# Kernel tuning notes

Measured on AMD Instinct MI355X. Metric: run time of the kernel, lower is better.

Reference implementation:

```python
import jax, jax.numpy as jnp
import numpy as np

EMB_DIM = 1024
N_HEADS = 16
HEAD_DIM = EMB_DIM // N_HEADS
B, T = 2, 2048


def setup_inputs() -> dict:
    key = jax.random.key(0)
    ks = jax.random.split(key, 5)
    scale = 1.0 / np.sqrt(EMB_DIM)
    x = jax.random.normal(ks[0], (B, T, EMB_DIM), dtype=jnp.float32)
    # causal mask: True means masked (as in torch masked_fill)
    mask = jnp.triu(jnp.ones((T, T), dtype=bool), k=1)[None, None, :, :]
    WQ = jax.random.normal(ks[1], (EMB_DIM, EMB_DIM), dtype=jnp.float32) * scale
    WK = jax.random.normal(ks[2], (EMB_DIM, EMB_DIM), dtype=jnp.float32) * scale
    WV = jax.random.normal(ks[3], (EMB_DIM, EMB_DIM), dtype=jnp.float32) * scale
    WO = jax.random.normal(ks[4], (EMB_DIM, EMB_DIM), dtype=jnp.float32) * scale
    return {"x": x, "mask": mask, "WQ": WQ, "WK": WK, "WV": WV, "WO": WO}


def reference(x, mask, WQ, WK, WV, WO):
    Bb, Tt, E = x.shape
    H, D = N_HEADS, HEAD_DIM

    def split(y):  # [B,T,E] -> [B,H,T,D]
        return y.reshape(Bb, Tt, H, D).transpose(0, 2, 1, 3)

    # nn.Linear(bias=False): y = x @ W.T with W of shape [out, in]
    Q = split(jnp.einsum('bte,oe->bto', x, WQ))
    K = split(jnp.einsum('bte,oe->bto', x, WK))
    V = split(jnp.einsum('bte,oe->bto', x, WV))

    scores = jnp.einsum('bhqd,bhkd->bhqk', Q, K) / jnp.sqrt(jnp.float32(D))
    scores = jnp.where(mask, -jnp.inf, scores)
    w = jax.nn.softmax(scores, axis=-1)
    w = jnp.nan_to_num(w, nan=0.0)  # fully-masked rows -> 0, as in torch
    out = jnp.einsum('bhqk,bhkd->bhqd', w, V)
    # dropout is identity at inference (eval mode)
    merged = out.transpose(0, 2, 1, 3).reshape(Bb, Tt, E)
    y = jnp.einsum('bte,oe->bto', merged, WO)
    return y, w
```

## Files before the change

kernel.cpp:

```cpp
#include <hip/hip_runtime.h>
#include <cstdint>
#include <cstddef>

typedef __attribute__((ext_vector_type(4))) float  f32x4;
typedef __attribute__((ext_vector_type(8))) short  s16x8;
typedef __attribute__((ext_vector_type(4))) short  s16x4;
typedef __attribute__((ext_vector_type(2))) unsigned int u32x2;

#define EMB   1024
#define NHEAD 16
#define HD    64
#define NB    2
#define TT    2048
#define TQKV  3072

#define C_EXP2 0.18033688011112042f

__device__ __forceinline__ short f2bf(float f) {
  union { float f; unsigned u; } x; x.f = f;
  unsigned r = x.u + 0x7FFFu + ((x.u >> 16) & 1u);
  return (short)(r >> 16);
}

__device__ __forceinline__ unsigned cvt_pk_bf16(float lo, float hi) {
  unsigned r;
  asm("v_cvt_pk_bf16_f32 %0, %1, %2" : "=v"(r) : "v"(lo), "v"(hi));
  return r;
}

__device__ __forceinline__ void gload_lds16(const short* g, short* l) {
  __builtin_amdgcn_global_load_lds(
      (const __attribute__((address_space(1))) void*)(g),
      (__attribute__((address_space(3))) void*)(l), 16, 0, 0);
}

__device__ __forceinline__ void bar_vm0() {
  asm volatile("s_waitcnt vmcnt(0)" ::: "memory");
  __builtin_amdgcn_sched_barrier(0);
  __builtin_amdgcn_s_barrier();
  __builtin_amdgcn_sched_barrier(0);
}
__device__ __forceinline__ void bar_vm1() {
  asm volatile("s_waitcnt vmcnt(1)" ::: "memory");
  __builtin_amdgcn_sched_barrier(0);
  __builtin_amdgcn_s_barrier();
  __builtin_amdgcn_sched_barrier(0);
}
__device__ __forceinline__ void bar_vm4() {
  asm volatile("s_waitcnt vmcnt(4)" ::: "memory");
  __builtin_amdgcn_sched_barrier(0);
  __builtin_amdgcn_s_barrier();
  __builtin_amdgcn_sched_barrier(0);
}

__global__ __launch_bounds__(256) void cvt_all(
    const float* __restrict__ x,  const float* __restrict__ wq,
    const float* __restrict__ wk, const float* __restrict__ wv,
    const float* __restrict__ wo,
    short* __restrict__ xb, short* __restrict__ wqkv, short* __restrict__ wob) {
  int i = blockIdx.x * 256 + threadIdx.x;
  const float* s; short* d; int off;
  if (i < 1048576) { s = x; d = xb; off = i; }
  else {
    int j = i - 1048576;
    int r = j >> 18;
    off = j & 262143;
    s = (r == 0) ? wq : (r == 1) ? wk : (r == 2) ? wv : wo;
    d = (r == 3) ? wob : wqkv + (size_t)r * 1048576;
  }
  f32x4 v = ((const f32x4*)s)[off];
  s16x4 o;
  o[0] = f2bf(v[0]); o[1] = f2bf(v[1]); o[2] = f2bf(v[2]); o[3] = f2bf(v[3]);
  ((s16x4*)d)[off] = o;
}

template <int OUT_BF16>
__global__ __launch_bounds__(512) void gemm_nt(const short* __restrict__ A,
                                               const short* __restrict__ B,
                                               void* __restrict__ C,
                                               int M, int N, int K) {
  __shared__ short lA[2][128 * 32];
  __shared__ short lB[2][128 * 32];
  const int tid  = threadIdx.x;
  const int lane = tid & 63;
  const int wid  = tid >> 6;
  const int bm = blockIdx.y, bn = blockIdx.x;
  const int wm = wid >> 2, wn = wid & 3;

  f32x4 acc[4][2];
#pragma unroll
  for (int i = 0; i < 4; ++i)
#pragma unroll
    for (int j = 0; j < 2; ++j) acc[i][j] = (f32x4){0.f, 0.f, 0.f, 0.f};

  const short* Ab = A + (size_t)bm * 128 * K;
  const short* Bb = B + (size_t)bn * 128 * K;
  const int srow = tid >> 2;
  const int scol = (((tid & 3) ^ (srow & 3))) * 8;

#define G_STAGE(buf, k0)                                                     \
  do {                                                                       \
    gload_lds16(Ab + (size_t)srow * K + (k0) + scol, &lA[buf][tid * 8]);     \
    gload_lds16(Bb + (size_t)srow * K + (k0) + scol, &lB[buf][tid * 8]);     \
  } while (0)

  G_STAGE(0, 0);
  int cur = 0;
  for (int k0 = 0; k0 < K; k0 += 32) {
    __syncthreads();
    if (k0 + 32 < K) G_STAGE(cur ^ 1, k0 + 32);

    s16x8 af[4], bf_[2];
#pragma unroll
    for (int i = 0; i < 4; ++i) {
      const int ra = wm * 64 + i * 16 + (lane & 15);
      af[i] = *(const s16x8*)(&lA[cur][ra * 32 + (((lane >> 4) ^ (ra & 3)) << 3)]);
    }
#pragma unroll
    for (int j = 0; j < 2; ++j) {
      const int rb = wn * 32 + j * 16 + (lane & 15);
      bf_[j] = *(const s16x8*)(&lB[cur][rb * 32 + (((lane >> 4) ^ (rb & 3)) << 3)]);
    }
#pragma unroll
    for (int i = 0; i < 4; ++i)
#pragma unroll
      for (int j = 0; j < 2; ++j)
        acc[i][j] = __builtin_amdgcn_mfma_f32_16x16x32_bf16(af[i], bf_[j], acc[i][j], 0, 0, 0);
    cur ^= 1;
  }
#undef G_STAGE

  const int row0 = bm * 128 + wm * 64;
  const int col0 = bn * 128 + wn * 32;
#pragma unroll
  for (int i = 0; i < 4; ++i)
#pragma unroll
    for (int j = 0; j < 2; ++j)
#pragma unroll
      for (int r = 0; r < 4; ++r) {
        int row = row0 + i * 16 + ((lane >> 4) << 2) + r;
        int col = col0 + j * 16 + (lane & 15);
        float v = acc[i][j][r];
        if (OUT_BF16) ((short*)C)[(size_t)row * N + col] = f2bf(v);
        else          ((float*)C)[(size_t)row * N + col] = v;
      }
}

__global__ __launch_bounds__(256) void transpose_v(const short* __restrict__ qkv,
                                                   short* __restrict__ vt) {
  __shared__ short tile[64 * 72];
  const int tt = blockIdx.x, bh = blockIdx.y;
  const int b = bh >> 4, h = bh & 15;
  const int tid = threadIdx.x;

  const short* src = qkv + ((size_t)(b * TT + tt * 64)) * TQKV + 2048 + h * HD;
#pragma unroll
  for (int p = 0; p < 2; ++p) {
    int r = p * 32 + (tid >> 3);
    int c = (tid & 7) * 8;
    s16x8 v = *(const s16x8*)(src + (size_t)r * TQKV + c);
#pragma unroll
    for (int j = 0; j < 8; ++j) tile[r * 72 + c + j] = v[j];
  }
  __syncthreads();
  short* dst = vt + ((size_t)bh * HD) * TT + tt * 64;
#pragma unroll
  for (int p = 0; p < 2; ++p) {
    int d0 = p * 32 + (tid >> 3);
    int c  = (tid & 7) * 8;
    s16x8 o;
#pragma unroll
    for (int j = 0; j < 8; ++j) o[j] = tile[(c + j) * 72 + d0];
    *(s16x8*)(dst + (size_t)d0 * TT + c) = o;
  }
}

__global__ __launch_bounds__(512) void attn_fused(const short* __restrict__ qkv,
                                                  const short* __restrict__ vt,
                                                  float* __restrict__ wout,
                                                  short* __restrict__ merged) {
  __shared__ short smem[28672];
  short* const lW  = smem;
  short* const lK0 = smem + 8192;
  short* const lK1 = smem + 12288;
  short* const lK2 = smem + 16384;
  short* const lV0 = smem + 20480;
  short* const lV1 = smem + 24576;

  const int tid = threadIdx.x, lane = tid & 63, wid = tid >> 6;
  const int bh = blockIdx.y;
  const int qt = (blockIdx.y < 16) ? (15 - blockIdx.x) : blockIdx.x;
  const int b = bh >> 4, h = bh & 15;
  const int NT = 2 * qt + 2;

  const int srow = tid >> 3;
  const int scol = ((tid & 7) ^ (srow & 7)) * 8;
  const int q15  = lane & 15;
  const int fcs  = (lane >> 4) * 8;
  const int kg4  = (lane >> 4) << 2;
  const int qg   = wid * 16 + q15;
  const int qglob = qt * 128 + qg;
  const int sw   = (q15 & 7) << 3;
  const int qsub = (lane >> 4) << 2;
  const int qrow = qt * 128 + wid * 16 + qsub;
  const int wave_qmin = qt * 128 + wid * 16;

  const short* ksrc0 = qkv + (size_t)(b * TT) * TQKV + EMB + h * HD;
  const short* vsrc0 = vt + (size_t)bh * HD * TT;

#define STAGE_K(dst, kt)                                                       \
  gload_lds16(ksrc0 + (size_t)((kt) * 64 + srow) * TQKV + scol, (dst) + tid * 8)
#define STAGE_V(dst, kt)                                                       \
  gload_lds16(vsrc0 + (size_t)srow * TT + (kt) * 64 + scol,     (dst) + tid * 8)

  const short* qsrc = qkv + ((size_t)(b * TT + qt * 128)) * TQKV + h * HD;
  gload_lds16(qsrc + (size_t)srow * TQKV + scol,        lW + tid * 8);
  gload_lds16(qsrc + (size_t)(srow + 64) * TQKV + scol, lW + 4096 + tid * 8);
  __syncthreads();

  s16x8 aq[2];
  aq[0] = *(const s16x8*)(lW + qg * 64 + ((fcs)      ^ ((qg & 7) << 3)));
  aq[1] = *(const s16x8*)(lW + qg * 64 + ((32 + fcs) ^ ((qg & 7) << 3)));

  float lsum = 0.f;
  {
    short *p0 = lK0, *p1 = lK1, *p2 = lK2;
    STAGE_K(p0, 0);
    STAGE_K(p1, 1);
    bar_vm0();
    for (int kt = 0; kt < NT; ++kt) {
      const bool pre = (kt + 2 < NT);
      if (pre) STAGE_K(p2, kt + 2);

      f32x4 s2[4];
#pragma unroll
      for (int kg = 0; kg < 4; ++kg) s2[kg] = (f32x4){0.f, 0.f, 0.f, 0.f};
#pragma unroll
      for (int ks2 = 0; ks2 < 2; ++ks2)
#pragma unroll
        for (int kg = 0; kg < 4; ++kg) {
          s16x8 bk = *(const s16x8*)(p0 + (kg * 16 + q15) * 64 + ((ks2 * 32 + fcs) ^ sw));
          s2[kg] = __builtin_amdgcn_mfma_f32_16x16x32_bf16(bk, aq[ks2], s2[kg], 0, 0, 0);
        }

      const bool full = (kt * 64 + 63 <= wave_qmin);
      const int kb0 = kt * 64 + kg4;
#pragma unroll
      for (int kg = 0; kg < 4; ++kg)
#pragma unroll
        for (int r = 0; r < 4; ++r) {
          float e = exp2f(s2[kg][r] * C_EXP2);
          if (!full) e = (kb0 + kg * 16 + r <= qglob) ? e : 0.f;
          lsum += e;
        }

      if (pre) bar_vm1();
      else     bar_vm0();
      short* t_ = p0; p0 = p1; p1 = p2; p2 = t_;
    }
  }
  lsum += __shfl_xor(lsum, 16);
  lsum += __shfl_xor(lsum, 32);
  const float lrl = -log2f(lsum);

  f32x4 o[4];
#pragma unroll
  for (int nj = 0; nj < 4; ++nj) o[nj] = (f32x4){0.f, 0.f, 0.f, 0.f};

  {
    short *kc_ = lK0, *kn_ = lK1, *vc_ = lV0, *vn_ = lV1;
    STAGE_K(kc_, 0);
    STAGE_V(vc_, 0);
    bar_vm0();
    float* const wq_base = wout + ((size_t)bh * TT + qglob) * TT;
    for (int kt = 0; kt < NT; ++kt) {
      f32x4 s2[4];
#pragma unroll
      for (int kg = 0; kg < 4; ++kg) s2[kg] = (f32x4){0.f, 0.f, 0.f, 0.f};
#pragma unroll
      for (int ks2 = 0; ks2 < 2; ++ks2)
#pragma unroll
        for (int kg = 0; kg < 4; ++kg) {
          s16x8 bk = *(const s16x8*)(kc_ + (kg * 16 + q15) * 64 + ((ks2 * 32 + fcs) ^ sw));
          s2[kg] = __builtin_amdgcn_mfma_f32_16x16x32_bf16(bk, aq[ks2], s2[kg], 0, 0, 0);
        }

      const bool pre = (kt + 1 < NT);
      if (pre) { STAGE_K(kn_, kt + 1); STAGE_V(vn_, kt + 1); }
      __builtin_amdgcn_sched_barrier(0);

      const bool full = (kt * 64 + 63 <= wave_qmin);
      float* wbase = wq_base + kt * 64 + kg4;
#pragma unroll
      for (int kg = 0; kg < 4; ++kg) {
        f32x4 w4;
#pragma unroll
        for (int r = 0; r < 4; ++r) {
          float e = exp2f(fmaf(s2[kg][r], C_EXP2, lrl));
          w4[r] = (full || (kt * 64 + kg * 16 + kg4 + r <= qglob)) ? e : 0.f;
        }
        *(f32x4*)(wbase + kg * 16) = w4;
        u32x2 pk2;
        pk2.x = cvt_pk_bf16(w4[0], w4[1]);
        pk2.y = cvt_pk_bf16(w4[2], w4[3]);
        const int col = kg * 16 + kg4;
        *(u32x2*)(lW + qg * 64 + (col ^ sw)) = pk2;
      }
      __builtin_amdgcn_sched_barrier(0);

#pragma unroll
      for (int ks2 = 0; ks2 < 2; ++ks2) {
        s16x8 aw = *(const s16x8*)(lW + qg * 64 + ((ks2 * 32 + fcs) ^ ((qg & 7) << 3)));
#pragma unroll
        for (int nj = 0; nj < 4; ++nj) {
          s16x8 bv = *(const s16x8*)(vc_ + (nj * 16 + q15) * 64 + ((ks2 * 32 + fcs) ^ sw));
          o[nj] = __builtin_amdgcn_mfma_f32_16x16x32_bf16(aw, bv, o[nj], 0, 0, 0);
        }
      }

      if (pre) {
        bar_vm4();
        short* t_;
        t_ = kc_; kc_ = kn_; kn_ = t_;
        t_ = vc_; vc_ = vn_; vn_ = t_;
      }
    }
  }
#undef STAGE_K
#undef STAGE_V

#pragma unroll
  for (int nj = 0; nj < 4; ++nj)
#pragma unroll
    for (int r = 0; r < 4; ++r)
      merged[(size_t)(b * TT + qrow + r) * EMB + h * HD + nj * 16 + q15] = f2bf(o[nj][r]);

  {
    const int zrow = tid >> 2, zc = (tid & 3) * 16;
    float* zbase = wout + ((size_t)bh * TT + qt * 128 + zrow) * TT + zc;
    const f32x4 z = (f32x4){0.f, 0.f, 0.f, 0.f};
    for (int kt = NT; kt < TT / 64; ++kt) {
      float* p = zbase + kt * 64;
      *(f32x4*)(p)      = z;
      *(f32x4*)(p + 4)  = z;
      *(f32x4*)(p + 8)  = z;
      *(f32x4*)(p + 12) = z;
    }
  }
}

extern "C" void kernel_launch(void* const* d_in, const int* in_sizes, int n_in,
                              void* d_out, int out_size, void* d_ws, size_t ws_size,
                              hipStream_t stream) {
  const float* x  = (const float*)d_in[0];
  const float* WQ = (const float*)d_in[2];
  const float* WK = (const float*)d_in[3];
  const float* WV = (const float*)d_in[4];
  const float* WO = (const float*)d_in[5];

  float* y    = (float*)d_out;
  float* wout = (float*)d_out + (size_t)NB * TT * EMB;

  char* ws = (char*)d_ws;
  short* xb     = (short*)(ws + 0);
  short* wqkv   = (short*)(ws + 8388608);
  short* wob    = (short*)(ws + 14680064);
  short* qkvb   = (short*)(ws + 16777216);
  short* vtb    = (short*)(ws + 41943040);
  short* merged = (short*)(ws + 50331648);

  cvt_all<<<8192, 256, 0, stream>>>(x, WQ, WK, WV, WO, xb, wqkv, wob);

  gemm_nt<1><<<dim3(24, 32), 512, 0, stream>>>(xb, wqkv, qkvb, 4096, 3072, 1024);

  transpose_v<<<dim3(32, 32), 256, 0, stream>>>(qkvb, vtb);

  attn_fused<<<dim3(16, 32), 512, 0, stream>>>(qkvb, vtb, wout, merged);

  gemm_nt<0><<<dim3(8, 32), 512, 0, stream>>>(merged, wob, y, 4096, 1024, 1024);
}
```

Measured before the change: 241.3 us.

## Process K/V tiles in pairs per barrier with deeper LDS buffering and setprio

Both attention passes now handle two 64-key tiles per loop iteration. LDS grows from three K and two V buffers to eight tile buffers, so that work is staged a pair at a time and each block hits half as many s_barrier and vmcnt waits. MFMA sections are wrapped in s_setprio to favour matrix issue across waves. In exchange, LDS use per block rises, which may cut occupancy. The waitcnt thresholds (vm2/vm4/vm8) depend on the order in which loads and stores retire, so the pipeline depth actually achieved may be smaller than intended.

```diff
diff --git a/kernel.cpp b/kernel.cpp
--- a/kernel.cpp
+++ b/kernel.cpp
@@ -34,24 +34,18 @@
       (__attribute__((address_space(3))) void*)(l), 16, 0, 0);
 }
 
-__device__ __forceinline__ void bar_vm0() {
-  asm volatile("s_waitcnt vmcnt(0)" ::: "memory");
-  __builtin_amdgcn_sched_barrier(0);
-  __builtin_amdgcn_s_barrier();
-  __builtin_amdgcn_sched_barrier(0);
-}
-__device__ __forceinline__ void bar_vm1() {
-  asm volatile("s_waitcnt vmcnt(1)" ::: "memory");
-  __builtin_amdgcn_sched_barrier(0);
-  __builtin_amdgcn_s_barrier();
-  __builtin_amdgcn_sched_barrier(0);
-}
-__device__ __forceinline__ void bar_vm4() {
-  asm volatile("s_waitcnt vmcnt(4)" ::: "memory");
-  __builtin_amdgcn_sched_barrier(0);
-  __builtin_amdgcn_s_barrier();
-  __builtin_amdgcn_sched_barrier(0);
-}
+#define MAKE_BAR(NAME, N)                                          \
+  __device__ __forceinline__ void NAME() {                         \
+    asm volatile("s_waitcnt vmcnt(" #N ")" ::: "memory");          \
+    __builtin_amdgcn_sched_barrier(0);                             \
+    __builtin_amdgcn_s_barrier();                                  \
+    __builtin_amdgcn_sched_barrier(0);                             \
+  }
+MAKE_BAR(bar_vm0, 0)
+MAKE_BAR(bar_vm2, 2)
+MAKE_BAR(bar_vm4, 4)
+MAKE_BAR(bar_vm8, 8)
+#undef MAKE_BAR
 
 __global__ __launch_bounds__(256) void cvt_all(
     const float* __restrict__ x,  const float* __restrict__ wq,
@@ -179,19 +173,16 @@
                                                   const short* __restrict__ vt,
                                                   float* __restrict__ wout,
                                                   short* __restrict__ merged) {
-  __shared__ short smem[28672];
-  short* const lW  = smem;
-  short* const lK0 = smem + 8192;
-  short* const lK1 = smem + 12288;
-  short* const lK2 = smem + 16384;
-  short* const lV0 = smem + 20480;
-  short* const lV1 = smem + 24576;
+  __shared__ short smem[40960];
+  short* const lW    = smem;
+  short* const tiles = smem + 8192;
+#define TB(i) (tiles + (i) * 4096)
 
   const int tid = threadIdx.x, lane = tid & 63, wid = tid >> 6;
   const int bh = blockIdx.y;
   const int qt = (blockIdx.y < 16) ? (15 - blockIdx.x) : blockIdx.x;
   const int b = bh >> 4, h = bh & 15;
-  const int NT = 2 * qt + 2;
+  const int npairs = qt + 1;
 
   const int srow = tid >> 3;
   const int scol = ((tid & 7) ^ (srow & 7)) * 8;
@@ -222,41 +213,55 @@
   aq[0] = *(const s16x8*)(lW + qg * 64 + ((fcs)      ^ ((qg & 7) << 3)));
   aq[1] = *(const s16x8*)(lW + qg * 64 + ((32 + fcs) ^ ((qg & 7) << 3)));
 
+#define QK_TILE(s2v, Kb)                                                       \
+  do {                                                                         \
+    _Pragma("unroll")                                                          \
+    for (int kg = 0; kg < 4; ++kg) s2v[kg] = (f32x4){0.f, 0.f, 0.f, 0.f};      \
+    __builtin_amdgcn_s_setprio(1);                                             \
+    _Pragma("unroll")                                                          \
+    for (int ks2 = 0; ks2 < 2; ++ks2)                                          \
+      _Pragma("unroll")                                                        \
+      for (int kg = 0; kg < 4; ++kg) {                                         \
+        s16x8 bk = *(const s16x8*)((Kb) + (kg * 16 + q15) * 64 +               \
+                                   ((ks2 * 32 + fcs) ^ sw));                   \
+        s2v[kg] = __builtin_amdgcn_mfma_f32_16x16x32_bf16(bk, aq[ks2],         \
+                                                          s2v[kg], 0, 0, 0);   \
+      }                                                                        \
+    __builtin_amdgcn_s_setprio(0);                                             \
+  } while (0)
+
   float lsum = 0.f;
   {
-    short *p0 = lK0, *p1 = lK1, *p2 = lK2;
-    STAGE_K(p0, 0);
-    STAGE_K(p1, 1);
-    bar_vm0();
-    for (int kt = 0; kt < NT; ++kt) {
-      const bool pre = (kt + 2 < NT);
-      if (pre) STAGE_K(p2, kt + 2);
-
-      f32x4 s2[4];
-#pragma unroll
-      for (int kg = 0; kg < 4; ++kg) s2[kg] = (f32x4){0.f, 0.f, 0.f, 0.f};
-#pragma unroll
-      for (int ks2 = 0; ks2 < 2; ++ks2)
-#pragma unroll
-        for (int kg = 0; kg < 4; ++kg) {
-          s16x8 bk = *(const s16x8*)(p0 + (kg * 16 + q15) * 64 + ((ks2 * 32 + fcs) ^ sw));
-          s2[kg] = __builtin_amdgcn_mfma_f32_16x16x32_bf16(bk, aq[ks2], s2[kg], 0, 0, 0);
-        }
-
-      const bool full = (kt * 64 + 63 <= wave_qmin);
-      const int kb0 = kt * 64 + kg4;
-#pragma unroll
-      for (int kg = 0; kg < 4; ++kg)
-#pragma unroll
-        for (int r = 0; r < 4; ++r) {
-          float e = exp2f(s2[kg][r] * C_EXP2);
-          if (!full) e = (kb0 + kg * 16 + r <= qglob) ? e : 0.f;
-          lsum += e;
-        }
-
-      if (pre) bar_vm1();
-      else     bar_vm0();
-      short* t_ = p0; p0 = p1; p1 = p2; p2 = t_;
+    STAGE_K(TB(0), 0); STAGE_K(TB(1), 1);
+    if (npairs > 1) { STAGE_K(TB(2), 2); STAGE_K(TB(3), 3); }
+    if (npairs > 1) bar_vm2(); else bar_vm0();
+    for (int p = 0; p < npairs; ++p) {
+      const int s = p & 3;
+      const bool pre = (p + 2 < npairs);
+      if (pre) {
+        const int sn = (p + 2) & 3;
+        STAGE_K(TB(2 * sn),     2 * p + 4);
+        STAGE_K(TB(2 * sn + 1), 2 * p + 5);
+      }
+      __builtin_amdgcn_sched_barrier(0);
+#pragma unroll
+      for (int u = 0; u < 2; ++u) {
+        const int t = 2 * p + u;
+        const short* Kb = TB(2 * s + u);
+        f32x4 s2v[4];
+        QK_TILE(s2v, Kb);
+        const bool full = (t * 64 + 63 <= wave_qmin);
+        const int kb0 = t * 64 + kg4;
+#pragma unroll
+        for (int kg = 0; kg < 4; ++kg)
+#pragma unroll
+          for (int r = 0; r < 4; ++r) {
+            float e = exp2f(s2v[kg][r] * C_EXP2);
+            if (!full) e = (kb0 + kg * 16 + r <= qglob) ? e : 0.f;
+            lsum += e;
+          }
+      }
+      if (p + 1 < npairs) { if (pre) bar_vm2(); else bar_vm0(); }
     }
   }
   lsum += __shfl_xor(lsum, 16);
@@ -267,67 +272,77 @@
 #pragma unroll
   for (int nj = 0; nj < 4; ++nj) o[nj] = (f32x4){0.f, 0.f, 0.f, 0.f};
 
+  __syncthreads();
   {
-    short *kc_ = lK0, *kn_ = lK1, *vc_ = lV0, *vn_ = lV1;
-    STAGE_K(kc_, 0);
-    STAGE_V(vc_, 0);
-    bar_vm0();
+    STAGE_K(TB(0), 0); STAGE_V(TB(1), 0); STAGE_K(TB(2), 1); STAGE_V(TB(3), 1);
+    if (npairs > 1) {
+      STAGE_K(TB(4), 2); STAGE_V(TB(5), 2); STAGE_K(TB(6), 3); STAGE_V(TB(7), 3);
+    }
+    if (npairs > 1) bar_vm4(); else bar_vm0();
+
     float* const wq_base = wout + ((size_t)bh * TT + qglob) * TT;
-    for (int kt = 0; kt < NT; ++kt) {
-      f32x4 s2[4];
-#pragma unroll
-      for (int kg = 0; kg < 4; ++kg) s2[kg] = (f32x4){0.f, 0.f, 0.f, 0.f};
-#pragma unroll
-      for (int ks2 = 0; ks2 < 2; ++ks2)
-#pragma unroll
-        for (int kg = 0; kg < 4; ++kg) {
-          s16x8 bk = *(const s16x8*)(kc_ + (kg * 16 + q15) * 64 + ((ks2 * 32 + fcs) ^ sw));
-          s2[kg] = __builtin_amdgcn_mfma_f32_16x16x32_bf16(bk, aq[ks2], s2[kg], 0, 0, 0);
-        }
-
-      const bool pre = (kt + 1 < NT);
-      if (pre) { STAGE_K(kn_, kt + 1); STAGE_V(vn_, kt + 1); }
-      __builtin_amdgcn_sched_barrier(0);
-
-      const bool full = (kt * 64 + 63 <= wave_qmin);
-      float* wbase = wq_base + kt * 64 + kg4;
-#pragma unroll
-      for (int kg = 0; kg < 4; ++kg) {
-        f32x4 w4;
-#pragma unroll
-        for (int r = 0; r < 4; ++r) {
-          float e = exp2f(fmaf(s2[kg][r], C_EXP2, lrl));
-          w4[r] = (full || (kt * 64 + kg * 16 + kg4 + r <= qglob)) ? e : 0.f;
-        }
-        *(f32x4*)(wbase + kg * 16) = w4;
-        u32x2 pk2;
-        pk2.x = cvt_pk_bf16(w4[0], w4[1]);
-        pk2.y = cvt_pk_bf16(w4[2], w4[3]);
-        const int col = kg * 16 + kg4;
-        *(u32x2*)(lW + qg * 64 + (col ^ sw)) = pk2;
+
+#define W_PV_TILE(s2v, t, Vb)                                                  \
+  do {                                                                         \
+    const bool full = ((t) * 64 + 63 <= wave_qmin);                            \
+    float* wbase = wq_base + (t) * 64 + kg4;                                   \
+    _Pragma("unroll")                                                          \
+    for (int kg = 0; kg < 4; ++kg) {                                           \
+      f32x4 w4;                                                                \
+      _Pragma("unroll")                                                        \
+      for (int r = 0; r < 4; ++r) {                                            \
+        float e = exp2f(fmaf(s2v[kg][r], C_EXP2, lrl));                        \
+        w4[r] = (full || ((t) * 64 + kg * 16 + kg4 + r <= qglob)) ? e : 0.f;   \
+      }                                                                        \
+      *(f32x4*)(wbase + kg * 16) = w4;                                         \
+      u32x2 pk2;                                                               \
+      pk2.x = cvt_pk_bf16(w4[0], w4[1]);                                       \
+      pk2.y = cvt_pk_bf16(w4[2], w4[3]);                                       \
+      const int col = kg * 16 + kg4;                                           \
+      *(u32x2*)(lW + qg * 64 + (col ^ sw)) = pk2;                              \
+    }                                                                          \
+    __builtin_amdgcn_s_setprio(1);                                             \
+    _Pragma("unroll")                                                          \
+    for (int ks2 = 0; ks2 < 2; ++ks2) {                                        \
+      s16x8 aw = *(const s16x8*)(lW + qg * 64 +                                \
+                                 ((ks2 * 32 + fcs) ^ ((qg & 7) << 3)));        \
+      _Pragma("unroll")                                                        \
+      for (int nj = 0; nj < 4; ++nj) {                                         \
+        s16x8 bv = *(const s16x8*)((Vb) + (nj * 16 + q15) * 64 +               \
+                                   ((ks2 * 32 + fcs) ^ sw));                   \
+        o[nj] = __builtin_amdgcn_mfma_f32_16x16x32_bf16(aw, bv, o[nj],         \
+                                                        0, 0, 0);              \
+      }                                                                        \
+    }                                                                          \
+    __builtin_amdgcn_s_setprio(0);                                             \
+  } while (0)
+
+    for (int p = 0; p < npairs; ++p) {
+      const int s = p & 1;
+      f32x4 s2v[4];
+      QK_TILE(s2v, TB(4 * s));
+
+      const bool st = (p >= 1 && p + 1 < npairs);
+      if (st) {
+        const int sn = (p + 1) & 1;
+        STAGE_K(TB(4 * sn),     2 * p + 2); STAGE_V(TB(4 * sn + 1), 2 * p + 2);
+        STAGE_K(TB(4 * sn + 2), 2 * p + 3); STAGE_V(TB(4 * sn + 3), 2 * p + 3);
       }
       __builtin_amdgcn_sched_barrier(0);
 
-#pragma unroll
-      for (int ks2 = 0; ks2 < 2; ++ks2) {
-        s16x8 aw = *(const s16x8*)(lW + qg * 64 + ((ks2 * 32 + fcs) ^ ((qg & 7) << 3)));
-#pragma unroll
-        for (int nj = 0; nj < 4; ++nj) {
-          s16x8 bv = *(const s16x8*)(vc_ + (nj * 16 + q15) * 64 + ((ks2 * 32 + fcs) ^ sw));
-          o[nj] = __builtin_amdgcn_mfma_f32_16x16x32_bf16(aw, bv, o[nj], 0, 0, 0);
-        }
-      }
-
-      if (pre) {
-        bar_vm4();
-        short* t_;
-        t_ = kc_; kc_ = kn_; kn_ = t_;
-        t_ = vc_; vc_ = vn_; vn_ = t_;
-      }
-    }
-  }
+      W_PV_TILE(s2v, 2 * p, TB(4 * s + 1));
+
+      QK_TILE(s2v, TB(4 * s + 2));
+      W_PV_TILE(s2v, 2 * p + 1, TB(4 * s + 3));
+
+      if (p + 1 < npairs) bar_vm8();
+    }
+#undef W_PV_TILE
+  }
+#undef QK_TILE
 #undef STAGE_K
 #undef STAGE_V
+#undef TB
 
 #pragma unroll
   for (int nj = 0; nj < 4; ++nj)
@@ -339,7 +354,7 @@
     const int zrow = tid >> 2, zc = (tid & 3) * 16;
     float* zbase = wout + ((size_t)bh * TT + qt * 128 + zrow) * TT + zc;
     const f32x4 z = (f32x4){0.f, 0.f, 0.f, 0.f};
-    for (int kt = NT; kt < TT / 64; ++kt) {
+    for (int kt = 2 * qt + 2; kt < TT / 64; ++kt) {
       float* p = zbase + kt * 64;
       *(f32x4*)(p)      = z;
       *(f32x4*)(p + 4)  = z;
```

After: 239.5 us. About the same (-0.7%).
